# Performance work log

Hardware: AMD Instinct MI355X
Metric: run time of the kernel (lower is better)

The kernel has to match this reference:

```python
import math
import jax, jax.numpy as jnp
import numpy as np

SCALES = (128.0, 256.0, 512.0)
ASPECT_RATIOS = (0.5, 1.0, 2.0)
NMS_THR = 0.7
PRENMS_K = 6000   # rpn_test_prenms_topk (module built with training=False)
POST_K = 300      # rpn_test_topk
MIN_SIZE = 16.0
DW_CLIP = math.log(1000.0 / 16.0)


def conv2d(x, w, b, pad):
    y = jax.lax.conv_general_dilated(
        x, w, window_strides=(1, 1), padding=[(pad, pad), (pad, pad)],
        dimension_numbers=("NCHW", "OIHW", "NCHW"))
    return y + b[None, :, None, None]


def generate_anchors(im_h, im_w, grid_h, grid_w, dtype):
    stride_h = float(im_h // grid_h)
    stride_w = float(im_w // grid_w)
    ar = jnp.asarray(ASPECT_RATIOS, dtype)
    sc = jnp.asarray(SCALES, dtype)
    h_ratios = jnp.sqrt(ar)
    w_ratios = 1.0 / h_ratios
    hs = (h_ratios[:, None] * sc[None, :]).reshape(-1)   # [A]
    ws = (w_ratios[:, None] * sc[None, :]).reshape(-1)
    base = jnp.round(jnp.stack([-ws, -hs, ws, hs], axis=1) / 2.0)  # [A,4]
    xs = jnp.arange(grid_w, dtype=dtype) * stride_w
    ys = jnp.arange(grid_h, dtype=dtype) * stride_h
    sy, sx = jnp.meshgrid(ys, xs, indexing="ij")
    sx = sx.reshape(-1); sy = sy.reshape(-1)
    shift = jnp.stack([sx, sy, sx, sy], axis=1)           # [HW,4]
    return (shift[:, None, :] + base[None, :, :]).reshape(-1, 4)  # [HW*A,4]


def decode_boxes(pred, anchors):
    # pred, anchors: [N,4] -> decoded [N,4]
    w = anchors[:, 2] - anchors[:, 0]
    h = anchors[:, 3] - anchors[:, 1]
    cx = anchors[:, 0] + 0.5 * w
    cy = anchors[:, 1] + 0.5 * h
    dx, dy = pred[:, 0], pred[:, 1]
    dw = jnp.minimum(pred[:, 2], DW_CLIP)
    dh = jnp.minimum(pred[:, 3], DW_CLIP)
    px = dx * w + cx
    py = dy * h + cy
    pw = jnp.exp(dw) * w
    ph = jnp.exp(dh) * h
    return jnp.stack([px - 0.5 * pw, py - 0.5 * ph, px + 0.5 * pw, py + 0.5 * ph], axis=1)


def nms_keep(boxes, valid, thr):
    # boxes assumed sorted by descending score; sequential greedy NMS.
    N = boxes.shape[0]
    area = (boxes[:, 2] - boxes[:, 0]) * (boxes[:, 3] - boxes[:, 1])
    idx = jnp.arange(N)

    def body(i, keep):
        b = jax.lax.dynamic_slice(boxes, (i, 0), (1, 4))[0]
        x1 = jnp.maximum(b[0], boxes[:, 0])
        y1 = jnp.maximum(b[1], boxes[:, 1])
        x2 = jnp.minimum(b[2], boxes[:, 2])
        y2 = jnp.minimum(b[3], boxes[:, 3])
        inter = jnp.clip(x2 - x1, 0.0) * jnp.clip(y2 - y1, 0.0)
        iou = inter / (area[i] + area - inter)
        suppress = (iou > thr) & (idx > i) & keep[i]
        return keep & ~suppress

    return jax.lax.fori_loop(0, N, body, valid)


def rpn_forward(image, feat, rpn_conv_w, rpn_conv_b, cls_w, cls_b, bbox_w, bbox_b):
    rpn_feat = jax.nn.relu(conv2d(feat, rpn_conv_w, rpn_conv_b, pad=1))
    cls_scores = conv2d(rpn_feat, cls_w, cls_b, pad=0)       # [B,A,H,W]
    box_pred = conv2d(rpn_feat, bbox_w, bbox_b, pad=0)       # [B,4A,H,W]
    B, A, H, W = cls_scores.shape
    im_h, im_w = image.shape[-2], image.shape[-1]
    anchors = generate_anchors(im_h, im_w, H, W, feat.dtype)  # [HWA,4]

    cls_flat = jnp.transpose(cls_scores, (0, 2, 3, 1)).reshape(-1)              # [B*H*W*A]
    pred = jnp.transpose(box_pred.reshape(B, A, 4, H, W), (0, 3, 4, 1, 2)).reshape(-1, 4)
    proposals = decode_boxes(pred, anchors)                   # [N,4]

    scores = jax.nn.sigmoid(cls_flat)
    top_scores, top_idx = jax.lax.top_k(scores, PRENMS_K)
    props = proposals[top_idx]                                # [K,4]
    # clamp to image boundary
    props = jnp.stack([
        jnp.clip(props[:, 0], 0.0, float(im_w)),
        jnp.clip(props[:, 1], 0.0, float(im_h)),
        jnp.clip(props[:, 2], 0.0, float(im_w)),
        jnp.clip(props[:, 3], 0.0, float(im_h))], axis=1)
    w = props[:, 2] - props[:, 0]
    h = props[:, 3] - props[:, 1]
    valid = (w >= MIN_SIZE) & (h >= MIN_SIZE)
    keep = nms_keep(props, valid, NMS_THR)                    # already score-sorted
    masked = jnp.where(keep, top_scores, -jnp.inf)
    final_scores, sel = jax.lax.top_k(masked, POST_K)
    final_boxes = props[sel]
    ok = jnp.isfinite(final_scores)
    final_boxes = jnp.where(ok[:, None], final_boxes, 0.0)
    final_scores = jnp.where(ok, final_scores, 0.0)
    return jnp.concatenate([final_boxes, final_scores[:, None]], axis=1)  # [POST_K,5]


def setup_inputs() -> dict:
    key = jax.random.key(0)
    ks = jax.random.split(key, 6)
    C, H, W, A = 256, 128, 128, 9
    IMH = IMW = 1024
    std = 0.01
    return {
        "image": jax.random.normal(ks[0], (1, 3, IMH, IMW), jnp.float32),
        "feat": jax.random.normal(ks[1], (1, C, H, W), jnp.float32),
        "rpn_conv_w": jax.random.normal(ks[2], (C, C, 3, 3), jnp.float32) * std,
        "rpn_conv_b": jnp.zeros((C,), jnp.float32),
        "cls_w": jax.random.normal(ks[3], (A, C, 1, 1), jnp.float32) * std,
        "cls_b": jnp.zeros((A,), jnp.float32),
        "bbox_w": jax.random.normal(ks[4], (4 * A, C, 1, 1), jnp.float32) * std,
        "bbox_b": jnp.zeros((4 * A,), jnp.float32),
    }


def reference(image, feat, rpn_conv_w, rpn_conv_b, cls_w, cls_b, bbox_w, bbox_b):
    return rpn_forward(image, feat, rpn_conv_w, rpn_conv_b, cls_w, cls_b, bbox_w, bbox_b)
```

## Files before the change

### kernel.cpp

```cpp
#include <hip/hip_runtime.h>

#define HW 128
#define NPIX 16384
#define CIN 256
#define NSC 147456
#define PRENMS 6000
#define POSTK 300
#define DW_CLIP_F 4.135166556742356f
#define MW 96
typedef unsigned long long ull;

__global__ void wt_kernel(const float* __restrict__ w, float* __restrict__ wt,
                          unsigned* __restrict__ zp, ull* __restrict__ vb) {
    int i = blockIdx.x * 256 + threadIdx.x;
    if (i < 2304 * 256) {
        int k = i >> 8, co = i & 255;
        wt[i] = w[co * 2304 + k];
    }
    if (i < 16384 + 65536 + 64) zp[i] = 0u;
    if (i < 94) vb[i] = 0ull;
}

__global__ __launch_bounds__(256) void conv3x3_half_kernel(
    const float* __restrict__ feat, const float* __restrict__ wt,
    float* __restrict__ part)
{
    __shared__ float in_s[16 * 340];
    const int tx = threadIdx.x;
    const int ty = threadIdx.y;
    const int x0 = blockIdx.x * 32;
    const int y0 = blockIdx.y * 8;
    const int h  = blockIdx.z >> 3;
    const int co0 = (blockIdx.z & 7) << 5;
    const int tid = ty * 32 + tx;

    const int yy1 = tid / 34, xx1 = tid - yy1 * 34;
    const int t2 = tid + 256;
    const int yy2 = t2 / 34, xx2 = t2 - yy2 * 34;
    const int gy1 = y0 + yy1 - 1, gx1 = x0 + xx1 - 1;
    const int gy2 = y0 + yy2 - 1, gx2 = x0 + xx2 - 1;
    const bool p1 = ((unsigned)gy1 < 128u) && ((unsigned)gx1 < 128u);
    const bool p2 = (tid < 84) && ((unsigned)gy2 < 128u) && ((unsigned)gx2 < 128u);
    const int a1 = p1 ? (gy1 * 128 + gx1) : 0;
    const int a2 = p2 ? (gy2 * 128 + gx2) : 0;

    float acc[32];
#pragma unroll
    for (int i = 0; i < 32; ++i) acc[i] = 0.f;

    const float* fh = feat + h * 128 * NPIX;
    const float* wh = wt + h * 128 * 9 * 256;

    for (int s = 0; s < 8; ++s) {
        __syncthreads();
        const float* fbase = fh + s * 16 * NPIX;
#pragma unroll
        for (int ci = 0; ci < 16; ++ci) {
            float t = fbase[ci * NPIX + a1];
            in_s[ci * 340 + tid] = p1 ? t : 0.f;
        }
        if (tid < 84) {
#pragma unroll
            for (int ci = 0; ci < 16; ++ci) {
                float t = fbase[ci * NPIX + a2];
                in_s[ci * 340 + 256 + tid] = p2 ? t : 0.f;
            }
        }
        __syncthreads();
        const float* ws0 = wh + s * 16 * 9 * 256 + co0;
#pragma unroll 2
        for (int ci = 0; ci < 16; ++ci) {
            const float* wrow = ws0 + ci * 9 * 256;
#pragma unroll
            for (int t = 0; t < 9; ++t) {
                const int ky = t / 3, kx = t - ky * 3;
                float v = in_s[ci * 340 + (ty + ky) * 34 + (tx + kx)];
                const float* wp = wrow + t * 256;
#pragma unroll
                for (int co = 0; co < 32; ++co)
                    acc[co] = fmaf(v, wp[co], acc[co]);
            }
        }
    }
    float* po = part + h * (CIN * NPIX) + co0 * NPIX + (y0 + ty) * 128 + (x0 + tx);
#pragma unroll
    for (int co = 0; co < 32; ++co)
        po[co * NPIX] = acc[co];
}

__global__ __launch_bounds__(256) void heads_kernel(
    const float* __restrict__ part, const float* __restrict__ conv_b,
    const float* __restrict__ cls_w, const float* __restrict__ cls_b,
    const float* __restrict__ bbox_w, const float* __restrict__ bbox_b,
    float* __restrict__ scores, float* __restrict__ bb)
{
    __shared__ float wl[256][48];
    const int tid = threadIdx.x;
    for (int e = tid; e < 256 * 48; e += 256) {
        int ci = e / 48, s = e - ci * 48;
        wl[ci][s] = (s < 9) ? cls_w[s * CIN + ci]
                  : (s < 45) ? bbox_w[(s - 9) * CIN + ci] : 0.f;
    }
    __syncthreads();

    const int lane = tid & 63;
    const int sg   = tid >> 6;
    const int p    = blockIdx.x * 64 + lane;
    const int s0   = sg * 12;
    const int ns   = (sg == 3) ? 9 : 12;

    float acc[12];
#pragma unroll
    for (int i = 0; i < 12; ++i) acc[i] = 0.f;

    const float* part1 = part + CIN * NPIX;
#pragma unroll 4
    for (int ci = 0; ci < CIN; ++ci) {
        float a = part[ci * NPIX + p];
        float c = part1[ci * NPIX + p];
        float v = fmaxf(a + c + conv_b[ci], 0.f);
        const float* wr = &wl[ci][s0];
#pragma unroll
        for (int j = 0; j < 12; ++j)
            acc[j] = fmaf(v, wr[j], acc[j]);
    }
    for (int j = 0; j < ns; ++j) {
        int s = s0 + j;
        if (s < 9) {
            float sc = acc[j] + cls_b[s];
            scores[p * 9 + s] = 1.0f / (1.0f + expf(-sc));
        } else {
            bb[(s - 9) * NPIX + p] = acc[j] + bbox_b[s - 9];
        }
    }
}

__global__ __launch_bounds__(1024) void hist1_kernel(const float* __restrict__ scores,
                                                     unsigned* __restrict__ hist1) {
    __shared__ unsigned h[16384];
    const int tid = threadIdx.x;
    for (int i = tid; i < 16384; i += 1024) h[i] = 0u;
    __syncthreads();
    for (int i = blockIdx.x * 1024 + tid; i < NSC; i += gridDim.x * 1024) {
        unsigned bits = __float_as_uint(scores[i]);
        atomicAdd(&h[bits >> 16], 1u);
    }
    __syncthreads();
    for (int i = tid; i < 16384; i += 1024) {
        unsigned c = h[i];
        if (c) atomicAdd(&hist1[i], c);
    }
}

__global__ __launch_bounds__(1024) void scan1_kernel(const unsigned* __restrict__ hist,
                                                     unsigned* __restrict__ meta) {
    __shared__ unsigned ssum[1024];
    const int t = threadIdx.x;
    unsigned local[16];
    unsigned s = 0;
#pragma unroll
    for (int i = 0; i < 16; ++i) { local[i] = hist[t * 16 + i]; s += local[i]; }
    ssum[t] = s;
    __syncthreads();
    for (int off = 1; off < 1024; off <<= 1) {
        unsigned v = ssum[t] + ((t + off < 1024) ? ssum[t + off] : 0u);
        __syncthreads();
        ssum[t] = v;
        __syncthreads();
    }
    unsigned run = ssum[t] - s;
#pragma unroll
    for (int i = 15; i >= 0; --i) {
        unsigned nb = run + local[i];
        if (nb >= (unsigned)PRENMS && run < (unsigned)PRENMS) {
            meta[1] = (unsigned)(t * 16 + i);
            meta[2] = run;
        }
        run = nb;
    }
}

__global__ void hist2_kernel(const float* __restrict__ scores, const unsigned* __restrict__ meta,
                             unsigned* __restrict__ hist2) {
    int i = blockIdx.x * 256 + threadIdx.x;
    if (i < NSC) {
        unsigned bits = __float_as_uint(scores[i]);
        if ((bits >> 16) == meta[1]) atomicAdd(&hist2[bits & 0xFFFFu], 1u);
    }
}

__global__ __launch_bounds__(1024) void scan2_kernel(const unsigned* __restrict__ hist2,
                                                     unsigned* __restrict__ meta) {
    __shared__ unsigned ssum[1024];
    const int t = threadIdx.x;
    const unsigned need = (unsigned)PRENMS - meta[2];
    unsigned s = 0;
    for (int i = 0; i < 64; ++i) s += hist2[t * 64 + i];
    ssum[t] = s;
    __syncthreads();
    for (int off = 1; off < 1024; off <<= 1) {
        unsigned v = ssum[t] + ((t + off < 1024) ? ssum[t + off] : 0u);
        __syncthreads();
        ssum[t] = v;
        __syncthreads();
    }
    unsigned run = ssum[t] - s;
    for (int i = 63; i >= 0; --i) {
        unsigned h = hist2[t * 64 + i];
        unsigned nb = run + h;
        if (nb >= need && run < need) {
            meta[3] = (meta[1] << 16) | (unsigned)(t * 64 + i);
        }
        run = nb;
    }
}

__global__ void compact_kernel(const float* __restrict__ scores, unsigned* __restrict__ meta,
                               ull* __restrict__ cand) {
    int i = blockIdx.x * 256 + threadIdx.x;
    unsigned bits = (i < NSC) ? __float_as_uint(scores[i]) : 0u;
    bool pred = (i < NSC) && (bits >= meta[3]);
    ull bal = __ballot(pred);
    int lane = threadIdx.x & 63;
    unsigned cnt = (unsigned)__popcll(bal);
    unsigned base = 0;
    if (lane == 0 && cnt) base = atomicAdd(&meta[0], cnt);
    base = __shfl(base, 0);
    if (pred) {
        unsigned off = (unsigned)__popcll(bal & ((1ull << lane) - 1ull));
        unsigned pos = base + off;
        if (pos < 8192u)
            cand[pos] = ((ull)bits << 32) | (unsigned)(~i);
    }
}

__global__ __launch_bounds__(1024) void sortA_kernel(const ull* __restrict__ cand,
                                                     const unsigned* __restrict__ meta,
                                                     ull* __restrict__ sorted) {
    __shared__ ull keys[2048];
    const int tid = threadIdx.x;
    const int base = blockIdx.x * 2048;
    const int n = min((int)meta[0], 8192);
    for (int i = tid; i < 2048; i += 1024) {
        int g = base + i;
        keys[i] = (g < n) ? cand[g] : (ull)(8191 - g);
    }
    __syncthreads();
    for (int k = 2; k <= 2048; k <<= 1) {
        for (int j = k >> 1; j >= 1; j >>= 1) {
            int s = tid;
            int i = ((s & ~(j - 1)) << 1) | (s & (j - 1));
            int p = i | j;
            ull a = keys[i], c = keys[p];
            bool desc = ((i & k) == 0);
            bool sw = desc ? (a < c) : (a > c);
            if (sw) { keys[i] = c; keys[p] = a; }
            __syncthreads();
        }
    }
    for (int i = tid; i < 2048; i += 1024) sorted[base + i] = keys[i];
}

__global__ __launch_bounds__(256) void merge_decode_kernel(
    const ull* __restrict__ sorted, const float* __restrict__ bb,
    float* __restrict__ selbox, float* __restrict__ selsc,
    ull* __restrict__ validbits)
{
    const int g = blockIdx.x * 256 + threadIdx.x;
    ull x = sorted[g];
    const int c = g >> 11;
    int rank = g & 2047;
#pragma unroll
    for (int cc = 0; cc < 4; ++cc) {
        if (cc == c) continue;
        const ull* arr = sorted + cc * 2048;
        int lo = 0, hi = 2048;
        while (lo < hi) { int mid = (lo + hi) >> 1; if (arr[mid] > x) lo = mid + 1; else hi = mid; }
        rank += lo;
    }
    if (rank < PRENMS) {
        const int r = rank;
        unsigned sbits = (unsigned)(x >> 32);
        unsigned idx = ~(unsigned)(x & 0xFFFFFFFFull);
        float score = __uint_as_float(sbits);
        int p = (int)(idx / 9u);
        int a = (int)(idx - (unsigned)p * 9u);
        int y = p >> 7, xx = p & 127;
        float d0 = bb[(a * 4 + 0) * NPIX + p];
        float d1 = bb[(a * 4 + 1) * NPIX + p];
        float d2 = bb[(a * 4 + 2) * NPIX + p];
        float d3 = bb[(a * 4 + 3) * NPIX + p];
        int ar_i = a / 3, sc_i = a - ar_i * 3;
        float arv = (ar_i == 0) ? 0.5f : ((ar_i == 1) ? 1.0f : 2.0f);
        float scv = (sc_i == 0) ? 128.f : ((sc_i == 1) ? 256.f : 512.f);
        float hr = sqrtf(arv);
        float wr = 1.0f / hr;
        float hs = hr * scv;
        float wsv = wr * scv;
        float bx1 = rintf(-wsv * 0.5f), by1 = rintf(-hs * 0.5f);
        float bx2 = rintf(wsv * 0.5f),  by2 = rintf(hs * 0.5f);
        float ax1 = xx * 8.f + bx1, ay1 = y * 8.f + by1;
        float ax2 = xx * 8.f + bx2, ay2 = y * 8.f + by2;
        float wa = ax2 - ax1, ha = ay2 - ay1;
        float cx = ax1 + 0.5f * wa, cy = ay1 + 0.5f * ha;
        float dw = fminf(d2, DW_CLIP_F), dh = fminf(d3, DW_CLIP_F);
        float px = d0 * wa + cx, py = d1 * ha + cy;
        float pw = expf(dw) * wa, ph = expf(dh) * ha;
        float x1 = px - 0.5f * pw, y1 = py - 0.5f * ph;
        float x2 = px + 0.5f * pw, y2 = py + 0.5f * ph;
        x1 = fminf(fmaxf(x1, 0.f), 1024.f);
        y1 = fminf(fmaxf(y1, 0.f), 1024.f);
        x2 = fminf(fmaxf(x2, 0.f), 1024.f);
        y2 = fminf(fmaxf(y2, 0.f), 1024.f);
        float bw = x2 - x1, bh = y2 - y1;
        bool valid = (bw >= 16.f) && (bh >= 16.f);
        selbox[r * 4 + 0] = x1; selbox[r * 4 + 1] = y1;
        selbox[r * 4 + 2] = x2; selbox[r * 4 + 3] = y2;
        selsc[r] = score;
        if (valid) atomicOr(&validbits[r >> 6], 1ull << (r & 63));
    }
}

__global__ __launch_bounds__(256) void maskbuild_kernel(
    const float* __restrict__ selbox, ull* __restrict__ mask)
{
    __shared__ float jb0[64], jb1[64], jb2[64], jb3[64];
    const int jw = blockIdx.y;
    const int tid = threadIdx.x;
    const int i = blockIdx.x * 256 + tid;
    if (jw * 64 + 63 < blockIdx.x * 256) {
        if (i < PRENMS) mask[(size_t)i * MW + jw] = 0ull;
        return;
    }
    if (tid < 64) {
        int j = jw * 64 + tid;
        float x1 = 0.f, y1 = 0.f, x2 = 0.f, y2 = 0.f;
        if (j < PRENMS) {
            x1 = selbox[j * 4 + 0]; y1 = selbox[j * 4 + 1];
            x2 = selbox[j * 4 + 2]; y2 = selbox[j * 4 + 3];
        }
        jb0[tid] = x1; jb1[tid] = y1; jb2[tid] = x2; jb3[tid] = y2;
    }
    __syncthreads();
    if (i >= PRENMS) return;
    const float ix1 = selbox[i * 4 + 0], iy1 = selbox[i * 4 + 1];
    const float ix2 = selbox[i * 4 + 2], iy2 = selbox[i * 4 + 3];
    const float iarea = (ix2 - ix1) * (iy2 - iy1);
    ull word = 0ull;
    for (int b = 0; b < 64; ++b) {
        int j = jw * 64 + b;
        float xx1 = fmaxf(ix1, jb0[b]);
        float yy1 = fmaxf(iy1, jb1[b]);
        float xx2 = fminf(ix2, jb2[b]);
        float yy2 = fminf(iy2, jb3[b]);
        float iw = fmaxf(xx2 - xx1, 0.f);
        float ih = fmaxf(yy2 - yy1, 0.f);
        float inter = iw * ih;
        float jarea = (jb2[b] - jb0[b]) * (jb3[b] - jb1[b]);
        float iou = inter / (iarea + jarea - inter);
        if (j > i && iou > 0.7f) word |= (1ull << b);
    }
    mask[(size_t)i * MW + jw] = word;
}

__global__ __launch_bounds__(64) void nms_scan_kernel(
    const ull* __restrict__ validbits,
    const ull* __restrict__ mask,
    const float* __restrict__ selbox, const float* __restrict__ selsc,
    float* __restrict__ out)
{
    __shared__ int kept[POSTK];
    const int l = threadIdx.x;
    ull supp0 = ~validbits[l];
    ull supp1 = (l < 30) ? ~validbits[64 + l] : ~0ull;
    int nk = 0;
    ull ownrow_next = mask[(size_t)l * MW + 0];
    for (int wi = 0; wi < 94 && nk < POSTK; ++wi) {
        ull ownrow = ownrow_next;
        if (wi < 93) ownrow_next = mask[(size_t)((wi + 1) * 64 + l) * MW + (wi + 1)];
        ull wsup = (wi < 64) ? __shfl(supp0, wi) : __shfl(supp1, wi - 64);
        ull active = ~wsup;
        if (!active) continue;
        ull keptbits = 0ull;
        while (active && nk < POSTK) {
            int b = __builtin_ctzll(active);
            keptbits |= (1ull << b);
            if (l == 0) kept[nk] = wi * 64 + b;
            nk++;
            ull rowb = __shfl(ownrow, b);
            ull gt = (b == 63) ? 0ull : (~0ull << (b + 1));
            active &= gt & ~rowb;
        }
        while (keptbits) {
            int b0 = __builtin_ctzll(keptbits); keptbits &= keptbits - 1;
            int b1 = -1, b2 = -1, b3 = -1;
            if (keptbits) { b1 = __builtin_ctzll(keptbits); keptbits &= keptbits - 1; }
            if (keptbits) { b2 = __builtin_ctzll(keptbits); keptbits &= keptbits - 1; }
            if (keptbits) { b3 = __builtin_ctzll(keptbits); keptbits &= keptbits - 1; }
            const ull* r0 = mask + (size_t)(wi * 64 + b0) * MW;
            ull t0a = r0[l], t0b = (l < 30) ? r0[64 + l] : 0ull;
            ull t1a = 0, t1b = 0, t2a = 0, t2b = 0, t3a = 0, t3b = 0;
            if (b1 >= 0) { const ull* r1 = mask + (size_t)(wi * 64 + b1) * MW; t1a = r1[l]; t1b = (l < 30) ? r1[64 + l] : 0ull; }
            if (b2 >= 0) { const ull* r2 = mask + (size_t)(wi * 64 + b2) * MW; t2a = r2[l]; t2b = (l < 30) ? r2[64 + l] : 0ull; }
            if (b3 >= 0) { const ull* r3 = mask + (size_t)(wi * 64 + b3) * MW; t3a = r3[l]; t3b = (l < 30) ? r3[64 + l] : 0ull; }
            supp0 |= t0a | t1a | t2a | t3a;
            supp1 |= t0b | t1b | t2b | t3b;
        }
    }
    __syncthreads();
    for (int r = l; r < POSTK; r += 64) {
        if (r < nk) {
            int i = kept[r];
            out[r * 5 + 0] = selbox[i * 4 + 0];
            out[r * 5 + 1] = selbox[i * 4 + 1];
            out[r * 5 + 2] = selbox[i * 4 + 2];
            out[r * 5 + 3] = selbox[i * 4 + 3];
            out[r * 5 + 4] = selsc[i];
        } else {
            out[r * 5 + 0] = 0.f; out[r * 5 + 1] = 0.f;
            out[r * 5 + 2] = 0.f; out[r * 5 + 3] = 0.f;
            out[r * 5 + 4] = 0.f;
        }
    }
}

extern "C" void kernel_launch(void* const* d_in, const int* in_sizes, int n_in,
                              void* d_out, int out_size, void* d_ws, size_t ws_size,
                              hipStream_t stream) {
    const float* feat    = (const float*)d_in[1];
    const float* conv_w  = (const float*)d_in[2];
    const float* conv_b  = (const float*)d_in[3];
    const float* cls_w   = (const float*)d_in[4];
    const float* cls_b   = (const float*)d_in[5];
    const float* bbox_w  = (const float*)d_in[6];
    const float* bbox_b  = (const float*)d_in[7];
    float* out = (float*)d_out;

    char* ws = (char*)d_ws;
    float*    part      = (float*)(ws + 0);
    float*    wt        = (float*)(ws + 33554432);
    float*    bb        = (float*)(ws + 35913728);
    float*    scores    = (float*)(ws + 38273024);
    unsigned* hist1     = (unsigned*)(ws + 38862848);
    unsigned* hist2     = (unsigned*)(ws + 38928384);
    unsigned* meta      = (unsigned*)(ws + 39190528);
    ull*      cand      = (ull*)(ws + 39190784);
    ull*      sorted    = (ull*)(ws + 39256320);
    ull*      fin       = (ull*)(ws + 39321856);
    float*    selbox    = (float*)(ws + 39387392);
    float*    selsc     = (float*)(ws + 39483648);
    ull*      validbits = (ull*)(ws + 39507712);
    ull*      mask      = (ull*)(ws + 39508480);
    (void)fin;

    wt_kernel<<<2304, 256, 0, stream>>>(conv_w, wt, hist1, validbits);
    conv3x3_half_kernel<<<dim3(4, 16, 16), dim3(32, 8), 0, stream>>>(feat, wt, part);
    heads_kernel<<<256, 256, 0, stream>>>(part, conv_b, cls_w, cls_b, bbox_w, bbox_b, scores, bb);
    hist1_kernel<<<64, 1024, 0, stream>>>(scores, hist1);
    scan1_kernel<<<1, 1024, 0, stream>>>(hist1, meta);
    hist2_kernel<<<(NSC + 255) / 256, 256, 0, stream>>>(scores, meta, hist2);
    scan2_kernel<<<1, 1024, 0, stream>>>(hist2, meta);
    compact_kernel<<<(NSC + 255) / 256, 256, 0, stream>>>(scores, meta, cand);
    sortA_kernel<<<4, 1024, 0, stream>>>(cand, meta, sorted);
    merge_decode_kernel<<<32, 256, 0, stream>>>(sorted, bb, selbox, selsc, validbits);
    maskbuild_kernel<<<dim3(24, 94), 256, 0, stream>>>(selbox, mask);
    nms_scan_kernel<<<1, 64, 0, stream>>>(validbits, mask, selbox, selsc, out);
}
```

Before: 530.6 us.

## Fuse top-k threshold scans, histograms and compaction into one single-block kernel

```diff
diff --git a/kernel.cpp b/kernel.cpp
--- a/kernel.cpp
+++ b/kernel.cpp
@@ -152,86 +152,130 @@
     }
 }
 
-__global__ __launch_bounds__(1024) void scan1_kernel(const unsigned* __restrict__ hist,
-                                                     unsigned* __restrict__ meta) {
-    __shared__ unsigned ssum[1024];
-    const int t = threadIdx.x;
-    unsigned local[16];
-    unsigned s = 0;
-#pragma unroll
-    for (int i = 0; i < 16; ++i) { local[i] = hist[t * 16 + i]; s += local[i]; }
-    ssum[t] = s;
-    __syncthreads();
-    for (int off = 1; off < 1024; off <<= 1) {
-        unsigned v = ssum[t] + ((t + off < 1024) ? ssum[t + off] : 0u);
+__global__ __launch_bounds__(1024) void topk_finish_kernel(
+    const float* __restrict__ scores, const unsigned* __restrict__ hist1,
+    unsigned* __restrict__ meta, ull* __restrict__ cand)
+{
+    __shared__ unsigned sh[1024];
+    __shared__ unsigned g2[256];
+    __shared__ unsigned res[8];
+    const int tid = threadIdx.x;
+
+    {
+        unsigned local[16];
+        unsigned s = 0;
+#pragma unroll
+        for (int i = 0; i < 16; ++i) { local[i] = hist1[tid * 16 + i]; s += local[i]; }
+        sh[tid] = s;
         __syncthreads();
-        ssum[t] = v;
+        for (int off = 1; off < 1024; off <<= 1) {
+            unsigned v = sh[tid] + ((tid + off < 1024) ? sh[tid + off] : 0u);
+            __syncthreads();
+            sh[tid] = v;
+            __syncthreads();
+        }
+        unsigned run = sh[tid] - s;
+#pragma unroll
+        for (int i = 15; i >= 0; --i) {
+            unsigned nb = run + local[i];
+            if (nb >= (unsigned)PRENMS && run < (unsigned)PRENMS) {
+                res[0] = (unsigned)(tid * 16 + i);
+                res[1] = run;
+            }
+            run = nb;
+        }
+    }
+    __syncthreads();
+    const unsigned m1 = res[0];
+    const unsigned need2 = (unsigned)PRENMS - res[1];
+    const uint4* s4 = (const uint4*)scores;
+
+    if (tid < 256) g2[tid] = 0u;
+    __syncthreads();
+    for (int i = tid; i < NSC / 4; i += 1024) {
+        uint4 v = s4[i];
+        if ((v.x >> 16) == m1) atomicAdd(&g2[(v.x >> 8) & 0xFF], 1u);
+        if ((v.y >> 16) == m1) atomicAdd(&g2[(v.y >> 8) & 0xFF], 1u);
+        if ((v.z >> 16) == m1) atomicAdd(&g2[(v.z >> 8) & 0xFF], 1u);
+        if ((v.w >> 16) == m1) atomicAdd(&g2[(v.w >> 8) & 0xFF], 1u);
+    }
+    __syncthreads();
+    {
+        unsigned hg = (tid < 256) ? g2[tid] : 0u;
         __syncthreads();
-    }
-    unsigned run = ssum[t] - s;
-#pragma unroll
-    for (int i = 15; i >= 0; --i) {
-        unsigned nb = run + local[i];
-        if (nb >= (unsigned)PRENMS && run < (unsigned)PRENMS) {
-            meta[1] = (unsigned)(t * 16 + i);
-            meta[2] = run;
-        }
-        run = nb;
-    }
-}
-
-__global__ void hist2_kernel(const float* __restrict__ scores, const unsigned* __restrict__ meta,
-                             unsigned* __restrict__ hist2) {
-    int i = blockIdx.x * 256 + threadIdx.x;
-    if (i < NSC) {
-        unsigned bits = __float_as_uint(scores[i]);
-        if ((bits >> 16) == meta[1]) atomicAdd(&hist2[bits & 0xFFFFu], 1u);
-    }
-}
-
-__global__ __launch_bounds__(1024) void scan2_kernel(const unsigned* __restrict__ hist2,
-                                                     unsigned* __restrict__ meta) {
-    __shared__ unsigned ssum[1024];
-    const int t = threadIdx.x;
-    const unsigned need = (unsigned)PRENMS - meta[2];
-    unsigned s = 0;
-    for (int i = 0; i < 64; ++i) s += hist2[t * 64 + i];
-    ssum[t] = s;
-    __syncthreads();
-    for (int off = 1; off < 1024; off <<= 1) {
-        unsigned v = ssum[t] + ((t + off < 1024) ? ssum[t + off] : 0u);
+        for (int off = 1; off < 256; off <<= 1) {
+            unsigned v = 0;
+            if (tid < 256) v = g2[tid] + ((tid + off < 256) ? g2[tid + off] : 0u);
+            __syncthreads();
+            if (tid < 256) g2[tid] = v;
+            __syncthreads();
+        }
+        if (tid < 256) {
+            unsigned above = g2[tid] - hg;
+            if (above < need2 && above + hg >= need2) {
+                res[2] = (unsigned)tid;
+                res[3] = need2 - above;
+            }
+        }
+    }
+    __syncthreads();
+    const unsigned gstar = res[2];
+    const unsigned need3 = res[3];
+    const unsigned pref = (m1 << 8) | gstar;
+
+    if (tid < 256) g2[tid] = 0u;
+    __syncthreads();
+    for (int i = tid; i < NSC / 4; i += 1024) {
+        uint4 v = s4[i];
+        if ((v.x >> 8) == pref) atomicAdd(&g2[v.x & 0xFF], 1u);
+        if ((v.y >> 8) == pref) atomicAdd(&g2[v.y & 0xFF], 1u);
+        if ((v.z >> 8) == pref) atomicAdd(&g2[v.z & 0xFF], 1u);
+        if ((v.w >> 8) == pref) atomicAdd(&g2[v.w & 0xFF], 1u);
+    }
+    __syncthreads();
+    {
+        unsigned hb = (tid < 256) ? g2[tid] : 0u;
         __syncthreads();
-        ssum[t] = v;
-        __syncthreads();
-    }
-    unsigned run = ssum[t] - s;
-    for (int i = 63; i >= 0; --i) {
-        unsigned h = hist2[t * 64 + i];
-        unsigned nb = run + h;
-        if (nb >= need && run < need) {
-            meta[3] = (meta[1] << 16) | (unsigned)(t * 64 + i);
-        }
-        run = nb;
-    }
-}
-
-__global__ void compact_kernel(const float* __restrict__ scores, unsigned* __restrict__ meta,
-                               ull* __restrict__ cand) {
-    int i = blockIdx.x * 256 + threadIdx.x;
-    unsigned bits = (i < NSC) ? __float_as_uint(scores[i]) : 0u;
-    bool pred = (i < NSC) && (bits >= meta[3]);
-    ull bal = __ballot(pred);
-    int lane = threadIdx.x & 63;
-    unsigned cnt = (unsigned)__popcll(bal);
-    unsigned base = 0;
-    if (lane == 0 && cnt) base = atomicAdd(&meta[0], cnt);
-    base = __shfl(base, 0);
-    if (pred) {
-        unsigned off = (unsigned)__popcll(bal & ((1ull << lane) - 1ull));
-        unsigned pos = base + off;
-        if (pos < 8192u)
-            cand[pos] = ((ull)bits << 32) | (unsigned)(~i);
-    }
+        for (int off = 1; off < 256; off <<= 1) {
+            unsigned v = 0;
+            if (tid < 256) v = g2[tid] + ((tid + off < 256) ? g2[tid + off] : 0u);
+            __syncthreads();
+            if (tid < 256) g2[tid] = v;
+            __syncthreads();
+        }
+        if (tid < 256) {
+            unsigned above = g2[tid] - hb;
+            if (above < need3 && above + hb >= need3) res[4] = (unsigned)tid;
+        }
+    }
+    __syncthreads();
+    const unsigned thr = (m1 << 16) | (gstar << 8) | res[4];
+
+    if (tid == 0) res[5] = 0u;
+    __syncthreads();
+    const int lane = tid & 63;
+    for (int i = tid; i < NSC / 4; i += 1024) {
+        uint4 v = s4[i];
+        unsigned b[4] = { v.x, v.y, v.z, v.w };
+#pragma unroll
+        for (int k = 0; k < 4; ++k) {
+            bool pred = b[k] >= thr;
+            ull bal = __ballot(pred);
+            unsigned cnt = (unsigned)__popcll(bal);
+            unsigned base = 0;
+            if (lane == 0 && cnt) base = atomicAdd(&res[5], cnt);
+            base = __shfl(base, 0);
+            if (pred) {
+                unsigned off = (unsigned)__popcll(bal & ((1ull << lane) - 1ull));
+                unsigned pos = base + off;
+                int gi = i * 4 + k;
+                if (pos < 8192u)
+                    cand[pos] = ((ull)b[k] << 32) | (unsigned)(~gi);
+            }
+        }
+    }
+    __syncthreads();
+    if (tid == 0) meta[0] = res[5];
 }
 
 __global__ __launch_bounds__(1024) void sortA_kernel(const ull* __restrict__ cand,
@@ -442,25 +486,19 @@
     float*    bb        = (float*)(ws + 35913728);
     float*    scores    = (float*)(ws + 38273024);
     unsigned* hist1     = (unsigned*)(ws + 38862848);
-    unsigned* hist2     = (unsigned*)(ws + 38928384);
     unsigned* meta      = (unsigned*)(ws + 39190528);
     ull*      cand      = (ull*)(ws + 39190784);
     ull*      sorted    = (ull*)(ws + 39256320);
-    ull*      fin       = (ull*)(ws + 39321856);
     float*    selbox    = (float*)(ws + 39387392);
     float*    selsc     = (float*)(ws + 39483648);
     ull*      validbits = (ull*)(ws + 39507712);
     ull*      mask      = (ull*)(ws + 39508480);
-    (void)fin;
 
     wt_kernel<<<2304, 256, 0, stream>>>(conv_w, wt, hist1, validbits);
     conv3x3_half_kernel<<<dim3(4, 16, 16), dim3(32, 8), 0, stream>>>(feat, wt, part);
     heads_kernel<<<256, 256, 0, stream>>>(part, conv_b, cls_w, cls_b, bbox_w, bbox_b, scores, bb);
     hist1_kernel<<<64, 1024, 0, stream>>>(scores, hist1);
-    scan1_kernel<<<1, 1024, 0, stream>>>(hist1, meta);
-    hist2_kernel<<<(NSC + 255) / 256, 256, 0, stream>>>(scores, meta, hist2);
-    scan2_kernel<<<1, 1024, 0, stream>>>(hist2, meta);
-    compact_kernel<<<(NSC + 255) / 256, 256, 0, stream>>>(scores, meta, cand);
+    topk_finish_kernel<<<1, 1024, 0, stream>>>(scores, hist1, meta, cand);
     sortA_kernel<<<4, 1024, 0, stream>>>(cand, meta, sorted);
     merge_decode_kernel<<<32, 256, 0, stream>>>(sorted, bb, selbox, selsc, validbits);
     maskbuild_kernel<<<dim3(24, 94), 256, 0, stream>>>(selbox, mask);
```

Measured after the change: 519.2 us, median of 2. 1.02x faster.
